# Optimization experiments

Hardware: AMD Instinct MI355X
Metric: run time of the kernel (lower is better)

Reference implementation:

```python
import jax, jax.numpy as jnp
import numpy as np

T, K, E, H, I = 1024, 2, 8, 2048, 768


def setup_inputs() -> dict:
    key = jax.random.key(0)
    k1, k2, k3, k4, k5 = jax.random.split(key, 5)
    hidden_states = jax.random.normal(k1, (T, H), dtype=jnp.float32)
    top_k_index = jax.random.randint(k2, (T, K), 0, E)
    logits = jax.random.normal(k3, (T, K), dtype=jnp.float32)
    top_k_weights = jax.nn.softmax(logits, axis=-1)  # realistic routing weights
    # Linear-style weights: gate_up [E, 2I, H], down [E, H, I]; scaled like trained params
    gate_up_proj = jax.random.normal(k4, (E, 2 * I, H), dtype=jnp.float32) * 0.02
    down_proj = jax.random.normal(k5, (E, H, I), dtype=jnp.float32) * 0.02
    return {
        "hidden_states": hidden_states,
        "top_k_index": top_k_index,
        "top_k_weights": top_k_weights,
        "gate_up_proj": gate_up_proj,
        "down_proj": down_proj,
    }


def reference(hidden_states, top_k_index, top_k_weights, gate_up_proj, down_proj):
    """Dense-dispatch MoE forward: same math as the per-expert 4-bit loop.

    For every token t and routed expert e (with routing weight w):
      gate, up = split(x_t @ Wgu_e^T); y_t += w * (silu(gate)*up) @ Wd_e^T
    Expressed densely over experts; non-routed (token, expert) pairs get a
    combine weight of 0, so they contribute nothing.
    """
    num_experts = gate_up_proj.shape[0]
    # combine[t, e] = sum_k w[t,k] * [top_k_index[t,k] == e]
    combine = jnp.sum(
        jax.nn.one_hot(top_k_index, num_experts, dtype=hidden_states.dtype)
        * top_k_weights[..., None],
        axis=1,
    )  # [T, E]
    # gate_up: [T, E, 2I]
    gu = jnp.einsum("th,eoh->teo", hidden_states, gate_up_proj)
    gate, up = jnp.split(gu, 2, axis=-1)
    h = jax.nn.silu(gate) * up  # [T, E, I]
    # fold combine weight in before the down projection (scalar per (t,e))
    h = h * combine[:, :, None]
    out = jnp.einsum("tei,ehi->th", h, down_proj)  # [T, H]
    return out.astype(hidden_states.dtype)
```

## Files before the change

kernel.cpp:

```cpp
#include <hip/hip_runtime.h>
#include <hip/hip_bf16.h>

#define T_TOK 1024
#define TOPK  2
#define NEXP  8
#define HDIM  2048
#define IDIM  768
#define MROW  384

typedef __attribute__((ext_vector_type(4))) float f32x4;
typedef __attribute__((ext_vector_type(8))) short bf16x8;
typedef __attribute__((ext_vector_type(8))) unsigned short u16x8;
typedef __attribute__((ext_vector_type(8))) __bf16 bfv8;

__device__ __forceinline__ bf16x8 cvt8(f32x4 v0, f32x4 v1) {
  bfv8 r;
#pragma unroll
  for (int j = 0; j < 4; ++j) { r[j] = (__bf16)v0[j]; r[4 + j] = (__bf16)v1[j]; }
  return __builtin_bit_cast(bf16x8, r);
}

__device__ __forceinline__ void gload_lds16(const void* g, void* l) {
  __builtin_amdgcn_global_load_lds(
      (const __attribute__((address_space(1))) unsigned int*)((unsigned long long)g),
      (__attribute__((address_space(3))) unsigned int*)(unsigned int)(unsigned long long)(l),
      16, 0, 0);
}


__global__ void k_gather(const int* __restrict__ idx, const float* __restrict__ wts,
                         int* __restrict__ cnt, int* __restrict__ tok,
                         float* __restrict__ wl, int* __restrict__ inv) {
  int g = blockIdx.x * 256 + threadIdx.x;
  int e = idx[g];
  float w = wts[g];
  int pos = atomicAdd(&cnt[e], 1);
  if (pos < 2048) { tok[e * 2048 + pos] = g; wl[e * 2048 + pos] = w; }
  inv[g] = (pos < MROW) ? (e * MROW + pos) : -1;
}

__global__ __launch_bounds__(256) void k_compact(const float* __restrict__ x,
                                                 const int* __restrict__ inv,
                                                 unsigned short* __restrict__ xe) {
  int pid = blockIdx.x;
  int iv = inv[pid];
  if (iv < 0) return;
  const float* src = x + (size_t)(pid >> 1) * HDIM;
  unsigned short* dst = xe + (size_t)iv * HDIM;
  int i = threadIdx.x * 8;
  f32x4 a = *(const f32x4*)(src + i);
  f32x4 b = *(const f32x4*)(src + i + 4);
  *(bf16x8*)(dst + i) = cvt8(a, b);
}

__global__ __launch_bounds__(256) void k_gate_up(
    const unsigned short* __restrict__ xe, const float* __restrict__ Wgu,
    const int* __restrict__ cnt, const float* __restrict__ wl,
    unsigned short* __restrict__ hb)
{
  const int b = blockIdx.x;
  const int e = b & 7;
  const int r = b >> 3;
  const int mt = r % 3;
  const int nb = r / 3;
  const int m0 = mt * 128;
  int cc = cnt[e]; if (cc > MROW) cc = MROW;
  if (m0 >= cc) return;
  const int col0 = nb * 32;

  __shared__ unsigned short sA[2][128 * 64];
  __shared__ unsigned short sB[2][64 * 64];
  __shared__ float sW[128];

  const int tid = threadIdx.x;
  const int lane = tid & 63, wid = tid >> 6;

  if (tid < 128) sW[tid] = (m0 + tid < cc) ? wl[e * 2048 + m0 + tid] : 0.f;

  const unsigned short* xeE = xe + ((size_t)e * MROW + m0) * HDIM;
  const unsigned short* aSrc[4];
  unsigned int aDstOff[4];
#pragma unroll
  for (int i = 0; i < 4; ++i) {
    int row = wid * 32 + i * 8 + (lane >> 3);
    int csrc = (lane & 7) ^ (row & 7);
    aSrc[i] = xeE + (size_t)row * HDIM + csrc * 8;
    aDstOff[i] = (unsigned)(wid * 32 + i * 8) * 64;
  }

  const int brow = tid >> 2, cq = (tid & 3);
  const int ocol = (brow < 32) ? (col0 + brow) : (IDIM + col0 + (brow - 32));
  const float* bSrc = Wgu + ((size_t)e * 2 * IDIM + ocol) * HDIM + cq * 16;
  unsigned int bDst[2];
#pragma unroll
  for (int c2 = 0; c2 < 2; ++c2)
    bDst[c2] = (unsigned)(brow * 64 + (((cq * 2 + c2) ^ (brow & 7)) * 8));

  const int fl = lane & 15, q = lane >> 4;
  const int wm = (wid >> 1) * 64, wn = (wid & 1) * 16;

  f32x4 accg[4], accu[4];
#pragma unroll
  for (int rf = 0; rf < 4; ++rf) {
    accg[rf] = f32x4{0.f, 0.f, 0.f, 0.f};
    accu[rf] = f32x4{0.f, 0.f, 0.f, 0.f};
  }

  f32x4 bl[4];

  auto STAGE_ISSUE = [&](int buf, int kt) {
#pragma unroll
    for (int i = 0; i < 4; ++i)
      gload_lds16(aSrc[i] + kt, &sA[buf][aDstOff[i]]);
#pragma unroll
    for (int j = 0; j < 4; ++j)
      bl[j] = *(const f32x4*)(bSrc + kt + j * 4);
  };
  auto STAGE_WRITE = [&](int buf) {
#pragma unroll
    for (int c2 = 0; c2 < 2; ++c2)
      *(bf16x8*)&sB[buf][bDst[c2]] = cvt8(bl[c2 * 2], bl[c2 * 2 + 1]);
  };
  auto COMPUTE = [&](int buf) {
    const unsigned short* A = sA[buf];
    const unsigned short* B = sB[buf];
#pragma unroll
    for (int s = 0; s < 2; ++s) {
      bf16x8 a[4], g2, u2;
#pragma unroll
      for (int rf = 0; rf < 4; ++rf) {
        int rr = wm + rf * 16 + fl;
        a[rf] = *(const bf16x8*)(A + rr * 64 + (((s * 4 + q) ^ (rr & 7)) * 8));
      }
      {
        int rg = wn + fl;
        g2 = *(const bf16x8*)(B + rg * 64 + (((s * 4 + q) ^ (rg & 7)) * 8));
        int ru = 32 + wn + fl;
        u2 = *(const bf16x8*)(B + ru * 64 + (((s * 4 + q) ^ (ru & 7)) * 8));
      }
#pragma unroll
      for (int rf = 0; rf < 4; ++rf) {
        accg[rf] = __builtin_amdgcn_mfma_f32_16x16x32_bf16(a[rf], g2, accg[rf], 0, 0, 0);
        accu[rf] = __builtin_amdgcn_mfma_f32_16x16x32_bf16(a[rf], u2, accu[rf], 0, 0, 0);
      }
    }
  };

  STAGE_ISSUE(0, 0);
  STAGE_WRITE(0);
  __syncthreads();
  int buf = 0;
  for (int kt = 0; kt < HDIM; kt += 64) {
    const int nxt = kt + 64;
    const bool more = nxt < HDIM;
    if (more) STAGE_ISSUE(buf ^ 1, nxt);
    COMPUTE(buf);
    if (more) STAGE_WRITE(buf ^ 1);
    __syncthreads();
    buf ^= 1;
  }

  unsigned short* hbE = hb + (size_t)e * MROW * IDIM;
  const int q4 = q * 4;
#pragma unroll
  for (int rf = 0; rf < 4; ++rf)
#pragma unroll
    for (int v = 0; v < 4; ++v) {
      int rowl = wm + rf * 16 + q4 + v;
      if (m0 + rowl < cc) {
        float g = accg[rf][v], u = accu[rf][v];
        float s = g / (1.f + __expf(-g));
        float h = s * u * sW[rowl];
        hbE[(size_t)(m0 + rowl) * IDIM + col0 + wn + fl] =
            __builtin_bit_cast(unsigned short, (__bf16)h);
      }
    }
}

__global__ __launch_bounds__(256, 3) void k_down(
    const unsigned short* __restrict__ hb, const float* __restrict__ Wd,
    const int* __restrict__ cnt, const int* __restrict__ tok,
    float* __restrict__ out)
{
  const int b = blockIdx.x;
  const int e = b & 7;
  const int r = b >> 3;
  const int mt = r % 6;
  const int nb = r / 6;
  const int m0 = mt * 64;
  int cc = cnt[e]; if (cc > MROW) cc = MROW;
  if (m0 >= cc) return;
  const int col0 = nb * 64;

  __shared__ unsigned short sA[3 * 4096];
  __shared__ unsigned short sB[3 * 4096];
  __shared__ int sTok[64];

  const int tid = threadIdx.x;
  const int lane = tid & 63, wid = tid >> 6;
  if (tid < 64) sTok[tid] = (m0 + tid < cc) ? (tok[e * 2048 + m0 + tid] >> 1) : 0;

  const unsigned short* hbE = hb + ((size_t)e * MROW + m0) * IDIM;
  const unsigned short* aSrc[2];
  unsigned int aDstOff[2];
#pragma unroll
  for (int i = 0; i < 2; ++i) {
    int row = wid * 16 + i * 8 + (lane >> 3);
    int csrc = (lane & 7) ^ (row & 7);
    aSrc[i] = hbE + (size_t)row * IDIM + csrc * 8;
    aDstOff[i] = (unsigned)(wid * 16 + i * 8) * 64;
  }

  const int brow = tid >> 2, cq = (tid & 3);
  const float* bSrc = Wd + ((size_t)e * HDIM + col0 + brow) * IDIM + cq * 16;
  unsigned int bDst[2];
#pragma unroll
  for (int c2 = 0; c2 < 2; ++c2)
    bDst[c2] = (unsigned)(brow * 64 + (((cq * 2 + c2) ^ (brow & 7)) * 8));

  const int fl = lane & 15, q = lane >> 4;
  const int wm = (wid >> 1) * 32, wn = (wid & 1) * 32;

  f32x4 acc[2][2];
#pragma unroll
  for (int mf = 0; mf < 2; ++mf)
#pragma unroll
    for (int nf = 0; nf < 2; ++nf) acc[mf][nf] = f32x4{0.f, 0.f, 0.f, 0.f};

  f32x4 blA[4], blB[4];
  const int NS = IDIM / 64;

  auto COMPUTE = [&](int bo) {
    const unsigned short* A = sA + bo;
    const unsigned short* B = sB + bo;
#pragma unroll
    for (int s = 0; s < 2; ++s) {
      bf16x8 a[2], bb[2];
#pragma unroll
      for (int mf = 0; mf < 2; ++mf) {
        int rr = wm + mf * 16 + fl;
        a[mf] = *(const bf16x8*)(A + rr * 64 + (((s * 4 + q) ^ (rr & 7)) * 8));
      }
#pragma unroll
      for (int nf = 0; nf < 2; ++nf) {
        int rn = wn + nf * 16 + fl;
        bb[nf] = *(const bf16x8*)(B + rn * 64 + (((s * 4 + q) ^ (rn & 7)) * 8));
      }
#pragma unroll
      for (int mf = 0; mf < 2; ++mf)
#pragma unroll
        for (int nf = 0; nf < 2; ++nf)
          acc[mf][nf] = __builtin_amdgcn_mfma_f32_16x16x32_bf16(a[mf], bb[nf], acc[mf][nf], 0, 0, 0);
    }
  };

  auto ITER = [&](int ks, f32x4 (&blR)[4], f32x4 (&blW)[4],
                  int oC, int oN, int oNN) {
    const bool nL = (ks + 2) < NS;
    const bool nW = (ks + 1) < NS;
    if (nL) {
#pragma unroll
      for (int i = 0; i < 2; ++i)
        gload_lds16(aSrc[i] + (ks + 2) * 64, &sA[oNN + aDstOff[i]]);
#pragma unroll
      for (int j = 0; j < 4; ++j)
        blW[j] = *(const f32x4*)(bSrc + (ks + 2) * 64 + j * 4);
    }
    if (nW) {
#pragma unroll
      for (int c2 = 0; c2 < 2; ++c2)
        *(bf16x8*)&sB[oN + bDst[c2]] = cvt8(blR[c2 * 2], blR[c2 * 2 + 1]);
    }
    COMPUTE(oC);
    if (nW) {
      if (nL) { asm volatile("s_waitcnt vmcnt(6) lgkmcnt(0)" ::: "memory"); }
      else    { asm volatile("s_waitcnt vmcnt(0) lgkmcnt(0)" ::: "memory"); }
      __builtin_amdgcn_sched_barrier(0);
      __builtin_amdgcn_s_barrier();
      __builtin_amdgcn_sched_barrier(0);
    }
  };

#pragma unroll
  for (int i = 0; i < 2; ++i) gload_lds16(aSrc[i], &sA[aDstOff[i]]);
#pragma unroll
  for (int j = 0; j < 4; ++j) blA[j] = *(const f32x4*)(bSrc + j * 4);
#pragma unroll
  for (int i = 0; i < 2; ++i) gload_lds16(aSrc[i] + 64, &sA[4096 + aDstOff[i]]);
#pragma unroll
  for (int j = 0; j < 4; ++j) blB[j] = *(const f32x4*)(bSrc + 64 + j * 4);
#pragma unroll
  for (int c2 = 0; c2 < 2; ++c2)
    *(bf16x8*)&sB[bDst[c2]] = cvt8(blA[c2 * 2], blA[c2 * 2 + 1]);
  asm volatile("s_waitcnt vmcnt(6) lgkmcnt(0)" ::: "memory");
  __builtin_amdgcn_sched_barrier(0);
  __builtin_amdgcn_s_barrier();
  __builtin_amdgcn_sched_barrier(0);

  int oC = 0, oN = 4096, oNN = 8192;
  for (int ks = 0; ks < NS; ks += 2) {
    ITER(ks, blB, blA, oC, oN, oNN);
    int t = oC; oC = oN; oN = oNN; oNN = t;
    ITER(ks + 1, blA, blB, oC, oN, oNN);
    t = oC; oC = oN; oN = oNN; oNN = t;
  }

  const int q4 = q * 4;
#pragma unroll
  for (int mf = 0; mf < 2; ++mf)
#pragma unroll
    for (int nf = 0; nf < 2; ++nf)
#pragma unroll
      for (int v = 0; v < 4; ++v) {
        int rowl = wm + mf * 16 + q4 + v;
        if (m0 + rowl < cc) {
          int t = sTok[rowl];
          atomicAdd(out + (size_t)t * HDIM + col0 + wn + nf * 16 + fl, acc[mf][nf][v]);
        }
      }
}

extern "C" void kernel_launch(void* const* d_in, const int* in_sizes, int n_in,
                              void* d_out, int out_size, void* d_ws, size_t ws_size,
                              hipStream_t stream) {
  const float* x   = (const float*)d_in[0];
  const int*   idx = (const int*)d_in[1];
  const float* wts = (const float*)d_in[2];
  const float* Wgu = (const float*)d_in[3];
  const float* Wd  = (const float*)d_in[4];
  float* out = (float*)d_out;

  char* ws = (char*)d_ws;
  int*            cnt = (int*)(ws + 0);
  int*            tok = (int*)(ws + 64);
  float*          wl  = (float*)(ws + 65600);
  int*            inv = (int*)(ws + 131136);
  unsigned short* xe  = (unsigned short*)(ws + 139328);
  unsigned short* hb  = (unsigned short*)(ws + 12722240);

  hipMemsetAsync(cnt, 0, NEXP * sizeof(int), stream);
  hipMemsetAsync(out, 0, (size_t)T_TOK * HDIM * sizeof(float), stream);
  k_gather<<<dim3((T_TOK * TOPK) / 256), 256, 0, stream>>>(idx, wts, cnt, tok, wl, inv);
  k_compact<<<dim3(T_TOK * TOPK), 256, 0, stream>>>(x, inv, xe);
  k_gate_up<<<dim3(NEXP * 3 * 24), 256, 0, stream>>>(xe, Wgu, cnt, wl, hb);
  k_down<<<dim3(NEXP * 6 * 32), 256, 0, stream>>>(hb, Wd, cnt, tok, out);
}
```

Measured before the change: 108.7 us.

## Triple-buffer gate_up GEMM with async LDS loads for fp32 weights

```diff
diff --git a/kernel.cpp b/kernel.cpp
--- a/kernel.cpp
+++ b/kernel.cpp
@@ -68,8 +68,8 @@
   if (m0 >= cc) return;
   const int col0 = nb * 32;
 
-  __shared__ unsigned short sA[2][128 * 64];
-  __shared__ unsigned short sB[2][64 * 64];
+  __shared__ unsigned short sA[3 * 4096];
+  __shared__ float          sB[3 * 2048];
   __shared__ float sW[128];
 
   const int tid = threadIdx.x;
@@ -78,23 +78,27 @@
   if (tid < 128) sW[tid] = (m0 + tid < cc) ? wl[e * 2048 + m0 + tid] : 0.f;
 
   const unsigned short* xeE = xe + ((size_t)e * MROW + m0) * HDIM;
-  const unsigned short* aSrc[4];
-  unsigned int aDstOff[4];
-#pragma unroll
-  for (int i = 0; i < 4; ++i) {
-    int row = wid * 32 + i * 8 + (lane >> 3);
-    int csrc = (lane & 7) ^ (row & 7);
+  const unsigned short* aSrc[2];
+  unsigned int aDstOff[2];
+#pragma unroll
+  for (int i = 0; i < 2; ++i) {
+    int row = wid * 32 + i * 16 + (lane >> 2);
+    int csrc = (lane & 3) ^ (row & 3);
     aSrc[i] = xeE + (size_t)row * HDIM + csrc * 8;
-    aDstOff[i] = (unsigned)(wid * 32 + i * 8) * 64;
-  }
-
-  const int brow = tid >> 2, cq = (tid & 3);
-  const int ocol = (brow < 32) ? (col0 + brow) : (IDIM + col0 + (brow - 32));
-  const float* bSrc = Wgu + ((size_t)e * 2 * IDIM + ocol) * HDIM + cq * 16;
-  unsigned int bDst[2];
-#pragma unroll
-  for (int c2 = 0; c2 < 2; ++c2)
-    bDst[c2] = (unsigned)(brow * 64 + (((cq * 2 + c2) ^ (brow & 7)) * 8));
+    aDstOff[i] = (unsigned)(wid * 32 + i * 16) * 32;
+  }
+
+  const float* bSrc[2];
+  unsigned int bDstOff[2];
+#pragma unroll
+  for (int i = 0; i < 2; ++i) {
+    int row = wid * 16 + i * 8 + (lane >> 3);
+    int c = lane & 7, h = c & 1, p = c >> 1;
+    int psrc = p ^ (row & 3);
+    int ocol = (row < 32) ? (col0 + row) : (IDIM + col0 + (row - 32));
+    bSrc[i] = Wgu + ((size_t)e * 2 * IDIM + ocol) * HDIM + psrc * 8 + h * 4;
+    bDstOff[i] = (unsigned)(wid * 16 + i * 8) * 32;
+  }
 
   const int fl = lane & 15, q = lane >> 4;
   const int wm = (wid >> 1) * 64, wn = (wid & 1) * 16;
@@ -106,58 +110,64 @@
     accu[rf] = f32x4{0.f, 0.f, 0.f, 0.f};
   }
 
-  f32x4 bl[4];
-
-  auto STAGE_ISSUE = [&](int buf, int kt) {
-#pragma unroll
-    for (int i = 0; i < 4; ++i)
-      gload_lds16(aSrc[i] + kt, &sA[buf][aDstOff[i]]);
-#pragma unroll
-    for (int j = 0; j < 4; ++j)
-      bl[j] = *(const f32x4*)(bSrc + kt + j * 4);
+  const int NS = HDIM / 32;
+
+  auto STAGE = [&](int step, int bo) {
+    const int kt = step * 32;
+#pragma unroll
+    for (int i = 0; i < 2; ++i)
+      gload_lds16(aSrc[i] + kt, &sA[bo * 4096 + aDstOff[i]]);
+#pragma unroll
+    for (int i = 0; i < 2; ++i)
+      gload_lds16(bSrc[i] + kt, &sB[bo * 2048 + bDstOff[i]]);
   };
-  auto STAGE_WRITE = [&](int buf) {
-#pragma unroll
-    for (int c2 = 0; c2 < 2; ++c2)
-      *(bf16x8*)&sB[buf][bDst[c2]] = cvt8(bl[c2 * 2], bl[c2 * 2 + 1]);
+
+  auto COMPUTE = [&](int bo) {
+    const unsigned short* A = sA + bo * 4096;
+    const float* B = sB + bo * 2048;
+    bf16x8 a[4];
+#pragma unroll
+    for (int rf = 0; rf < 4; ++rf) {
+      int rr = wm + rf * 16 + fl;
+      a[rf] = *(const bf16x8*)(A + rr * 32 + ((q ^ (rr & 3)) * 8));
+    }
+    bf16x8 g2, u2;
+    {
+      int rg = wn + fl;
+      const float* pg = B + rg * 32 + ((q ^ (rg & 3)) * 8);
+      g2 = cvt8(*(const f32x4*)pg, *(const f32x4*)(pg + 4));
+      int ru = 32 + wn + fl;
+      const float* pu = B + ru * 32 + ((q ^ (ru & 3)) * 8);
+      u2 = cvt8(*(const f32x4*)pu, *(const f32x4*)(pu + 4));
+    }
+#pragma unroll
+    for (int rf = 0; rf < 4; ++rf) {
+      accg[rf] = __builtin_amdgcn_mfma_f32_16x16x32_bf16(a[rf], g2, accg[rf], 0, 0, 0);
+      accu[rf] = __builtin_amdgcn_mfma_f32_16x16x32_bf16(a[rf], u2, accu[rf], 0, 0, 0);
+    }
   };
-  auto COMPUTE = [&](int buf) {
-    const unsigned short* A = sA[buf];
-    const unsigned short* B = sB[buf];
-#pragma unroll
-    for (int s = 0; s < 2; ++s) {
-      bf16x8 a[4], g2, u2;
-#pragma unroll
-      for (int rf = 0; rf < 4; ++rf) {
-        int rr = wm + rf * 16 + fl;
-        a[rf] = *(const bf16x8*)(A + rr * 64 + (((s * 4 + q) ^ (rr & 7)) * 8));
-      }
-      {
-        int rg = wn + fl;
-        g2 = *(const bf16x8*)(B + rg * 64 + (((s * 4 + q) ^ (rg & 7)) * 8));
-        int ru = 32 + wn + fl;
-        u2 = *(const bf16x8*)(B + ru * 64 + (((s * 4 + q) ^ (ru & 7)) * 8));
-      }
-#pragma unroll
-      for (int rf = 0; rf < 4; ++rf) {
-        accg[rf] = __builtin_amdgcn_mfma_f32_16x16x32_bf16(a[rf], g2, accg[rf], 0, 0, 0);
-        accu[rf] = __builtin_amdgcn_mfma_f32_16x16x32_bf16(a[rf], u2, accu[rf], 0, 0, 0);
-      }
-    }
-  };
-
-  STAGE_ISSUE(0, 0);
-  STAGE_WRITE(0);
-  __syncthreads();
-  int buf = 0;
-  for (int kt = 0; kt < HDIM; kt += 64) {
-    const int nxt = kt + 64;
-    const bool more = nxt < HDIM;
-    if (more) STAGE_ISSUE(buf ^ 1, nxt);
-    COMPUTE(buf);
-    if (more) STAGE_WRITE(buf ^ 1);
-    __syncthreads();
-    buf ^= 1;
+
+  STAGE(0, 0);
+  STAGE(1, 1);
+  asm volatile("s_waitcnt vmcnt(4)" ::: "memory");
+  __builtin_amdgcn_sched_barrier(0);
+  __builtin_amdgcn_s_barrier();
+  __builtin_amdgcn_sched_barrier(0);
+
+  int oC = 0, oN = 1, oNN = 2;
+#pragma unroll 1
+  for (int i = 0; i < NS; ++i) {
+    const bool st = (i + 2) < NS;
+    if (st) STAGE(i + 2, oNN);
+    COMPUTE(oC);
+    if (i < NS - 1) {
+      if (st) { asm volatile("s_waitcnt vmcnt(4)" ::: "memory"); }
+      else    { asm volatile("s_waitcnt vmcnt(0)" ::: "memory"); }
+      __builtin_amdgcn_sched_barrier(0);
+      __builtin_amdgcn_s_barrier();
+      __builtin_amdgcn_sched_barrier(0);
+    }
+    int t = oC; oC = oN; oN = oNN; oNN = t;
   }
 
   unsigned short* hbE = hb + (size_t)e * MROW * IDIM;
```

Measured after the change: 105.2 us. 1.03x faster.
